# Kernel tuning notes

Hardware: AMD Instinct MI355X
Metric: run time of the kernel (lower is better)

## Reference

```python
import jax, jax.numpy as jnp
import numpy as np

# ---- static config (mirrors SynthesisLayer __init__ with chosen init_kwargs) ----
B, CIN, COUT, H, W, WDIM = 8, 512, 512, 64, 64, 512
K = 3                      # conv_kernel (not torgb)
UP, DOWN = 2, 2            # tmp_fs=128 vs in/out fs=64
TAPS = 12                  # filter_size * factor
PX0, PX1, PY0, PY1 = 9, 8, 9, 8   # from the padding formula in __init__
CLAMP = 256.0
SLOPE = 0.2
LRELU_GAIN = float(np.sqrt(2.0))
IN_CUTOFF, IN_HALFW = 16.0, 16.0
OUT_CUTOFF, OUT_HALFW = 16.0, 16.0
TMP_FS = 128.0


def _design_lowpass(numtaps, cutoff, width, fs):
    # numpy re-implementation of scipy.signal.firwin (Kaiser-window design)
    nyq = fs / 2.0
    m = np.arange(numtaps) - (numtaps - 1) / 2.0
    c = cutoff / nyq
    h = c * np.sinc(c * m)
    atten = 2.285 * (numtaps - 1) * np.pi * (width / nyq) + 7.95  # kaiser_atten
    if atten > 50:
        beta = 0.1102 * (atten - 8.7)
    elif atten > 21:
        beta = 0.5842 * (atten - 21) ** 0.4 + 0.07886 * (atten - 21)
    else:
        beta = 0.0
    h *= np.kaiser(numtaps, beta)
    h /= h.sum()
    return jnp.asarray(h, dtype=jnp.float32)


def _upfirdn2d_sep(x, f, up=1, down=1, padding=(0, 0, 0, 0), gain=1.0):
    # separable 1D filter applied along W then H; matches NVIDIA upfirdn2d ref
    C = x.shape[1]
    px0, px1, py0, py1 = padding
    f = f[::-1]  # flip_filter=False -> true convolution
    f = (f * np.sqrt(gain)).astype(x.dtype)  # gain ** (ndim/2) per 1D pass
    k = f.shape[0]
    dn = ('NCHW', 'OIHW', 'NCHW')
    # zero-upsample (trailing zeros) == lhs_dilation + (up-1) extra high pad
    kw = jnp.tile(f.reshape(1, 1, 1, k), (C, 1, 1, 1))
    x = jax.lax.conv_general_dilated(x, kw, (1, down), ((0, 0), (px0, px1 + up - 1)),
                                     lhs_dilation=(1, up), dimension_numbers=dn,
                                     feature_group_count=C)
    kh = jnp.tile(f.reshape(1, 1, k, 1), (C, 1, 1, 1))
    x = jax.lax.conv_general_dilated(x, kh, (down, 1), ((py0, py1 + up - 1), (0, 0)),
                                     lhs_dilation=(up, 1), dimension_numbers=dn,
                                     feature_group_count=C)
    return x


def _modulated_conv2d(x, w, s):
    # demodulate=True path; input_gain = rsqrt(magnitude_ema=1) = 1
    b, i, h, wid = x.shape
    o = w.shape[0]
    w = w * jax.lax.rsqrt(jnp.mean(jnp.square(w), axis=(1, 2, 3), keepdims=True))
    s = s * jax.lax.rsqrt(jnp.mean(jnp.square(s)))
    wb = w[None] * s[:, None, :, None, None]                      # [B,O,I,kh,kw]
    d = jax.lax.rsqrt(jnp.sum(jnp.square(wb), axis=(2, 3, 4)) + 1e-8)  # [B,O]
    wb = wb * d[:, :, None, None, None]
    xg = x.reshape(1, b * i, h, wid)
    wg = wb.reshape(b * o, i, K, K)
    y = jax.lax.conv_general_dilated(xg, wg, (1, 1), ((K - 1, K - 1), (K - 1, K - 1)),
                                     dimension_numbers=('NCHW', 'OIHW', 'NCHW'),
                                     feature_group_count=b)
    return y.reshape(b, o, h + K - 1, wid + K - 1)


def setup_inputs() -> dict:
    key = jax.random.key(0)
    ks = jax.random.split(key, 5)
    x = jax.random.normal(ks[0], (B, CIN, H, W), jnp.float32)
    w_lat = jax.random.normal(ks[1], (B, WDIM), jnp.float32)
    conv_w = jax.random.normal(ks[2], (COUT, CIN, K, K), jnp.float32)
    conv_b = jax.random.normal(ks[3], (COUT,), jnp.float32) * 0.1
    aff_w = jax.random.normal(ks[4], (CIN, WDIM), jnp.float32)
    aff_b = jnp.ones((CIN,), jnp.float32)  # style affine bias_init=1
    up_f = _design_lowpass(TAPS, IN_CUTOFF, 2 * IN_HALFW, TMP_FS)
    dn_f = _design_lowpass(TAPS, OUT_CUTOFF, 2 * OUT_HALFW, TMP_FS)
    return {"x": x, "w_lat": w_lat, "conv_w": conv_w, "conv_b": conv_b,
            "aff_w": aff_w, "aff_b": aff_b, "up_f": up_f, "dn_f": dn_f}


def reference(x, w_lat, conv_w, conv_b, aff_w, aff_b, up_f, dn_f):
    # affine (equalized linear, weight scale 1/sqrt(w_dim))
    styles = (w_lat @ aff_w.T) * (1.0 / np.sqrt(WDIM)) + aff_b
    y = _modulated_conv2d(x, conv_w, styles)                     # [B,O,66,66]
    # filtered_lrelu reference: bias -> clamp -> FIR up -> lrelu*gain -> clamp -> FIR down
    y = y + conv_b[None, :, None, None]
    y = jnp.clip(y, -CLAMP, CLAMP)
    y = _upfirdn2d_sep(y, up_f, up=UP, padding=(PX0, PX1, PY0, PY1), gain=UP * UP)
    y = jax.nn.leaky_relu(y, SLOPE) * LRELU_GAIN
    y = jnp.clip(y, -CLAMP, CLAMP)
    y = _upfirdn2d_sep(y, dn_f, down=DOWN)                       # [B,O,64,64]
    return y
```

## Files before the change

kernel.cpp:

```cpp
#include <hip/hip_runtime.h>
#include <stdint.h>

typedef short short8 __attribute__((ext_vector_type(8)));
typedef float f32x4 __attribute__((ext_vector_type(4)));

__device__ __forceinline__ unsigned short f2bf(float f) {
  union { float f; unsigned u; } v; v.f = f;
  unsigned u = v.u;
  u += 0x7fffu + ((u >> 16) & 1u);
  return (unsigned short)(u >> 16);
}

__device__ __forceinline__ void gl16(const void* g, void* l) {
  __builtin_amdgcn_global_load_lds(
      (__attribute__((address_space(1))) void*)(uintptr_t)g,
      (__attribute__((address_space(3))) void*)l, 16, 0, 0);
}

#define NSPAT 36992
#define PLANE 4624
#define XHP_ROWS 37152

__global__ void styles_kernel(const float* __restrict__ w_lat, const float* __restrict__ affw,
                              const float* __restrict__ affb, float* __restrict__ s) {
  int g = blockIdx.x * 256 + threadIdx.x;
  int b = g >> 9, i = g & 511;
  const float4* wl = (const float4*)(w_lat + b * 512);
  const float4* aw = (const float4*)(affw + (size_t)i * 512);
  float acc = 0.f;
#pragma unroll 4
  for (int j = 0; j < 128; ++j) {
    float4 a = wl[j], c = aw[j];
    acc += a.x * c.x + a.y * c.y + a.z * c.z + a.w * c.w;
  }
  s[g] = acc * 0.044194173824159216f + affb[i];
}

__global__ void norm_kernel(float* __restrict__ s, float* __restrict__ s2) {
  __shared__ float red[256];
  int t = threadIdx.x;
  float acc = 0.f;
  for (int e = t; e < 4096; e += 256) { float v = s[e]; acc += v * v; }
  red[t] = acc; __syncthreads();
  for (int st = 128; st > 0; st >>= 1) {
    if (t < st) red[t] += red[t + st];
    __syncthreads();
  }
  float alpha = rsqrtf(red[0] * (1.0f / 4096.0f));
  for (int e = t; e < 4096; e += 256) {
    float v = s[e] * alpha;
    s[e] = v; s2[e] = v * v;
  }
}

__global__ void rowscale_kernel(const float* __restrict__ convw, float* __restrict__ rowscale) {
  int o = blockIdx.x, t = threadIdx.x;
  const float* wr = convw + (size_t)o * 4608;
  float acc = 0.f;
  for (int e = t; e < 4608; e += 256) { float v = wr[e]; acc += v * v; }
  __shared__ float red[256];
  red[t] = acc; __syncthreads();
  for (int st = 128; st > 0; st >>= 1) {
    if (t < st) red[t] += red[t + st];
    __syncthreads();
  }
  if (t == 0) rowscale[o] = rsqrtf(red[0] * (1.0f / 4608.0f));
}

__global__ void wprep_kernel(const float* __restrict__ convw, const float* __restrict__ rowscale,
                             unsigned short* __restrict__ wbf, float* __restrict__ W2) {
  int o = blockIdx.x, t = threadIdx.x;
  float sc = rowscale[o];
  for (int i = t; i < 512; i += 256) {
    const float* wp = convw + ((size_t)o * 512 + i) * 9;
    float w9[9]; float ss = 0.f;
#pragma unroll
    for (int m = 0; m < 9; ++m) { float v = wp[m] * sc; w9[m] = v; ss += v * v; }
    W2[((size_t)o << 9) + i] = ss;
#pragma unroll
    for (int m = 0; m < 9; ++m)
      wbf[(((size_t)m * 512 + o) << 9) + i] = f2bf(w9[m]);
  }
}

__global__ void demod_kernel(const float* __restrict__ s2, const float* __restrict__ W2,
                             float* __restrict__ dbuf) {
  int g = blockIdx.x * 256 + threadIdx.x;
  int b = g >> 9, o = g & 511;
  const float4* sp = (const float4*)(s2 + b * 512);
  const float4* wp = (const float4*)(W2 + (size_t)o * 512);
  float acc = 1e-8f;
#pragma unroll 4
  for (int j = 0; j < 128; ++j) {
    float4 a = sp[j], c = wp[j];
    acc += a.x * c.x + a.y * c.y + a.z * c.z + a.w * c.w;
  }
  dbuf[g] = rsqrtf(acc);
}

__global__ void xprep_kernel(const float* __restrict__ x, const float* __restrict__ s,
                             unsigned short* __restrict__ xhp) {
  int b = blockIdx.x >> 6, h = blockIdx.x & 63;
  int t = threadIdx.x;
  __shared__ float tile[64 * 65];
  __shared__ float sv[64];
  for (int it = 0; it < 8; ++it) {
    int i0 = it * 64;
    {
      int ii = t >> 2, wseg = (t & 3) * 16;
      const float4* src = (const float4*)(x + (((size_t)(b * 512 + i0 + ii) * 64 + h) << 6) + wseg);
      float4 v0 = src[0], v1 = src[1], v2 = src[2], v3 = src[3];
      float* dst = tile + ii * 65 + wseg;
      dst[0]=v0.x; dst[1]=v0.y; dst[2]=v0.z; dst[3]=v0.w;
      dst[4]=v1.x; dst[5]=v1.y; dst[6]=v1.z; dst[7]=v1.w;
      dst[8]=v2.x; dst[9]=v2.y; dst[10]=v2.z; dst[11]=v2.w;
      dst[12]=v3.x; dst[13]=v3.y; dst[14]=v3.z; dst[15]=v3.w;
    }
    if (t < 64) sv[t] = s[b * 512 + i0 + t];
    __syncthreads();
    {
      int w = t >> 2, ic = (t & 3) * 16;
      alignas(16) unsigned short tmp[16];
#pragma unroll
      for (int k = 0; k < 16; ++k)
        tmp[k] = f2bf(tile[(ic + k) * 65 + w] * sv[ic + k]);
      unsigned short* dst = xhp + ((size_t)b * PLANE + (h + 2) * 68 + (w + 2)) * 512 + i0 + ic;
      *(short8*)dst = *(const short8*)tmp;
      *(short8*)(dst + 8) = *(const short8*)(tmp + 8);
    }
    __syncthreads();
  }
}

__global__ __launch_bounds__(256, 3) void conv_kernel(const unsigned short* __restrict__ wbf,
                                                      const unsigned short* __restrict__ xhp,
                                                      const float* __restrict__ dbuf,
                                                      const float* __restrict__ convb,
                                                      float* __restrict__ ybuf) {
  __shared__ unsigned short lds[24576];
  const int t = threadIdx.x;
  const int lane = t & 63, wid = t >> 6;

  int orig = blockIdx.y * 4 + blockIdx.x;
  int xcd = orig & 7, idx = orig >> 3;
  int wg = (xcd < 4) ? (xcd * 145 + idx) : (580 + (xcd - 4) * 144 + idx);
  const int n0 = (wg >> 2) * 128, o0 = (wg & 3) * 128;
  const int wm = wid >> 1, wn = wid & 1;

  const unsigned kc = (((unsigned)(lane & 3)) ^ ((unsigned)(lane >> 3) & 3u)) * 8u;
  const unsigned aOff0 = (unsigned)(o0 + wid * 32 + (lane >> 2)) * 512 + kc;
  const unsigned aOff1 = aOff0 + 16 * 512;
  const unsigned bOff0 = (unsigned)(n0 + wid * 32 + (lane >> 2)) * 512 + kc;
  const unsigned bOff1 = bOff0 + 16 * 512;

  const unsigned xq = ((unsigned)(lane >> 4)) ^ (((unsigned)(lane & 15) >> 1) & 3u);
  const unsigned aFo = wm * 2048 + (lane & 15) * 32 + xq * 8;
  const unsigned bFo = 4096 + wn * 2048 + (lane & 15) * 32 + xq * 8;

  f32x4 acc[4][4] = {};

#define STAGE(stp, off) do {                                           \
    const unsigned tp = (unsigned)(stp) >> 4;                          \
    const unsigned k0 = ((unsigned)(stp) & 15u) * 32u;                 \
    const unsigned aT = tp * 262144u + k0;                             \
    const unsigned bS = ((tp / 3u) * 68u + (tp % 3u)) * 512u + k0;     \
    unsigned short* la = lds + (off) + wid * 1024;                     \
    unsigned short* lb = lds + (off) + 4096 + wid * 1024;              \
    gl16(wbf + aT + aOff0, la);                                        \
    gl16(wbf + aT + aOff1, la + 512);                                  \
    gl16(xhp + bS + bOff0, lb);                                        \
    gl16(xhp + bS + bOff1, lb + 512);                                  \
  } while (0)

#define COMPUTE(rdoff) do {                                            \
    const unsigned short* aF = lds + (rdoff) + aFo;                    \
    const unsigned short* bF = lds + (rdoff) + bFo;                    \
    short8 a0 = *(const short8*)(aF + 0);                              \
    short8 a1 = *(const short8*)(aF + 512);                            \
    short8 a2 = *(const short8*)(aF + 1024);                           \
    short8 a3 = *(const short8*)(aF + 1536);                           \
    short8 b0 = *(const short8*)(bF + 0);                              \
    short8 b1 = *(const short8*)(bF + 512);                            \
    short8 b2 = *(const short8*)(bF + 1024);                           \
    short8 b3 = *(const short8*)(bF + 1536);                           \
    __builtin_amdgcn_s_setprio(1);                                     \
    acc[0][0] = __builtin_amdgcn_mfma_f32_16x16x32_bf16(a0, b0, acc[0][0], 0, 0, 0); \
    acc[0][1] = __builtin_amdgcn_mfma_f32_16x16x32_bf16(a0, b1, acc[0][1], 0, 0, 0); \
    acc[0][2] = __builtin_amdgcn_mfma_f32_16x16x32_bf16(a0, b2, acc[0][2], 0, 0, 0); \
    acc[0][3] = __builtin_amdgcn_mfma_f32_16x16x32_bf16(a0, b3, acc[0][3], 0, 0, 0); \
    acc[1][0] = __builtin_amdgcn_mfma_f32_16x16x32_bf16(a1, b0, acc[1][0], 0, 0, 0); \
    acc[1][1] = __builtin_amdgcn_mfma_f32_16x16x32_bf16(a1, b1, acc[1][1], 0, 0, 0); \
    acc[1][2] = __builtin_amdgcn_mfma_f32_16x16x32_bf16(a1, b2, acc[1][2], 0, 0, 0); \
    acc[1][3] = __builtin_amdgcn_mfma_f32_16x16x32_bf16(a1, b3, acc[1][3], 0, 0, 0); \
    acc[2][0] = __builtin_amdgcn_mfma_f32_16x16x32_bf16(a2, b0, acc[2][0], 0, 0, 0); \
    acc[2][1] = __builtin_amdgcn_mfma_f32_16x16x32_bf16(a2, b1, acc[2][1], 0, 0, 0); \
    acc[2][2] = __builtin_amdgcn_mfma_f32_16x16x32_bf16(a2, b2, acc[2][2], 0, 0, 0); \
    acc[2][3] = __builtin_amdgcn_mfma_f32_16x16x32_bf16(a2, b3, acc[2][3], 0, 0, 0); \
    acc[3][0] = __builtin_amdgcn_mfma_f32_16x16x32_bf16(a3, b0, acc[3][0], 0, 0, 0); \
    acc[3][1] = __builtin_amdgcn_mfma_f32_16x16x32_bf16(a3, b1, acc[3][1], 0, 0, 0); \
    acc[3][2] = __builtin_amdgcn_mfma_f32_16x16x32_bf16(a3, b2, acc[3][2], 0, 0, 0); \
    acc[3][3] = __builtin_amdgcn_mfma_f32_16x16x32_bf16(a3, b3, acc[3][3], 0, 0, 0); \
    __builtin_amdgcn_s_setprio(0);                                     \
  } while (0)

  STAGE(0, 0u);
  STAGE(1, 8192u);

  unsigned rd = 0, wr2 = 16384;
  for (int step = 0; step < 143; ++step) {
    asm volatile("s_waitcnt vmcnt(4)" ::: "memory");
    __builtin_amdgcn_s_barrier();
    asm volatile("" ::: "memory");
    if (step < 142) STAGE(step + 2, wr2);
    COMPUTE(rd);
    asm volatile("" ::: "memory");
    rd += 8192;  if (rd == 24576) rd = 0;
    wr2 += 8192; if (wr2 == 24576) wr2 = 0;
  }
  asm volatile("s_waitcnt vmcnt(0)" ::: "memory");
  __builtin_amdgcn_s_barrier();
  asm volatile("" ::: "memory");
  COMPUTE(rd);
#undef STAGE
#undef COMPUTE

  const int col = lane & 15;
  const int rbase = (lane >> 4) * 4;
#pragma unroll
  for (int ni = 0; ni < 4; ++ni) {
    const unsigned n = (unsigned)(n0 + wn * 64 + ni * 16 + col);
    const unsigned b = n / 4624u;
    const float* dr = dbuf + b * 512;
#pragma unroll
    for (int mi = 0; mi < 4; ++mi) {
      const int ob = o0 + wm * 64 + mi * 16 + rbase;
#pragma unroll
      for (int j = 0; j < 4; ++j) {
        const int o = ob + j;
        float v = acc[mi][ni][j] * dr[o] + convb[o];
        v = fminf(fmaxf(v, -256.f), 256.f);
        ybuf[(size_t)o * NSPAT + n] = v;
      }
    }
  }
}

__global__ __launch_bounds__(256, 4) void updown_kernel(const float* __restrict__ ybuf,
                                                        const float* __restrict__ upf,
                                                        const float* __restrict__ dnf,
                                                        float* __restrict__ out) {
  __shared__ float sm[9880];
  float* uhB = sm;
  float* uB  = sm + 5016;
  float* dvT = sm + 5016;

  const int blk = blockIdx.x;
  const int half = blk & 1, ch = blk >> 1;
  const int o = ch & 511, b = ch >> 9;
  const float* ybase = ybuf + (size_t)o * NSPAT + b * PLANE;
  const int t = threadIdx.x;
  const int uc0 = half * 32 - 4;

  float f2[12], g[12];
#pragma unroll
  for (int m = 0; m < 12; ++m) { f2[m] = upf[11 - m] * 2.0f; g[m] = dnf[11 - m]; }

  for (int u = t; u < 726; u += 256) {
    int p = u / 11, q = u - p * 11;
    int gc = uc0 + 4 * q;
    f32x4 v = {0.f, 0.f, 0.f, 0.f};
    if (gc >= 0 && gc < 66) {
      v = *(const f32x4*)(ybase + p * 68 + gc);
#pragma unroll
      for (int j = 0; j < 4; ++j)
        if (gc + j >= 66) v[j] = 0.f;
    }
    *(f32x4*)(uB + p * 44 + 4 * q) = v;
  }
  __syncthreads();

  for (int u = t; u < 1254; u += 256) {
    int p = u / 19, cq = u - p * 19;
    const float* ur = uB + p * 44 + 2 * cq;
    float R0 = ur[0], R1 = ur[1], R2 = ur[2], R3 = ur[3], R4 = ur[4], R5 = ur[5], R6 = ur[6];
    f32x4 o4;
    o4[0] = f2[1]*R0 + f2[3]*R1 + f2[5]*R2 + f2[7]*R3 + f2[9]*R4 + f2[11]*R5;
    o4[1] = f2[0]*R0 + f2[2]*R1 + f2[4]*R2 + f2[6]*R3 + f2[8]*R4 + f2[10]*R5;
    o4[2] = f2[1]*R1 + f2[3]*R2 + f2[5]*R3 + f2[7]*R4 + f2[9]*R5 + f2[11]*R6;
    o4[3] = f2[0]*R1 + f2[2]*R2 + f2[4]*R3 + f2[6]*R4 + f2[8]*R5 + f2[10]*R6;
    *(f32x4*)(uhB + p * 76 + 4 * cq) = o4;
  }
  __syncthreads();

  if (t < 225) {
    const int cl = t % 75, sg = t / 75;
    const int s0 = sg * 22;
    const int ttg0 = 2 * s0;
    float R[32];
#pragma unroll
    for (int k = 0; k < 32; ++k) {
      int j = s0 - 4 + k;
      R[k] = (j >= 0 && j < 66) ? uhB[j * 76 + cl] : 0.f;
    }
    float dv[22];
#pragma unroll
    for (int m = 0; m < 22; ++m) dv[m] = 0.f;
#pragma unroll
    for (int k = 0; k < 54; ++k) {
      const int kb = k >> 1;
      float z;
      if (k & 1)
        z = f2[0]*R[kb] + f2[2]*R[kb+1] + f2[4]*R[kb+2] + f2[6]*R[kb+3] + f2[8]*R[kb+4] + f2[10]*R[kb+5];
      else
        z = f2[1]*R[kb] + f2[3]*R[kb+1] + f2[5]*R[kb+2] + f2[7]*R[kb+3] + f2[9]*R[kb+4] + f2[11]*R[kb+5];
      z = (z > 0.f ? z : 0.2f * z) * 1.4142135623730951f;
      z = fminf(fmaxf(z, -256.f), 256.f);
      if (ttg0 + k >= 138) z = 0.f;
      const int mlo = (k < 11) ? 0 : ((k - 10) >> 1);
      const int mhi = ((k >> 1) < 21) ? (k >> 1) : 21;
#pragma unroll
      for (int m = mlo; m <= mhi; ++m)
        dv[m] += g[k - 2 * m] * z;
    }
#pragma unroll
    for (int m = 0; m < 22; ++m) {
      const int s = s0 + m;
      if (s < 64) dvT[s * 76 + cl] = dv[m];
    }
  }
  __syncthreads();

  {
    const int s = t >> 2, rq = t & 3;
    const float* dr = dvT + s * 76 + 16 * rq;
    f32x4 dd[7];
#pragma unroll
    for (int i = 0; i < 7; ++i) dd[i] = *(const f32x4*)(dr + 4 * i);
    float D[28];
#pragma unroll
    for (int i = 0; i < 7; ++i) {
      D[4*i+0] = dd[i][0]; D[4*i+1] = dd[i][1]; D[4*i+2] = dd[i][2]; D[4*i+3] = dd[i][3];
    }
    f32x4 o0, o1;
#pragma unroll
    for (int m = 0; m < 8; ++m) {
      float v = g[0]*D[2*m] + g[1]*D[2*m+1] + g[2]*D[2*m+2] + g[3]*D[2*m+3]
              + g[4]*D[2*m+4] + g[5]*D[2*m+5] + g[6]*D[2*m+6] + g[7]*D[2*m+7]
              + g[8]*D[2*m+8] + g[9]*D[2*m+9] + g[10]*D[2*m+10] + g[11]*D[2*m+11];
      if (m < 4) o0[m] = v; else o1[m - 4] = v;
    }
    float* ob = out + (((size_t)(b * 512 + o)) << 12) + s * 64 + half * 32 + 8 * rq;
    *(f32x4*)ob = o0;
    *(f32x4*)(ob + 4) = o1;
  }
}

extern "C" void kernel_launch(void* const* d_in, const int* in_sizes, int n_in,
                              void* d_out, int out_size, void* d_ws, size_t ws_size,
                              hipStream_t stream) {
  const float* x     = (const float*)d_in[0];
  const float* w_lat = (const float*)d_in[1];
  const float* convw = (const float*)d_in[2];
  const float* convb = (const float*)d_in[3];
  const float* affw  = (const float*)d_in[4];
  const float* affb  = (const float*)d_in[5];
  const float* upf   = (const float*)d_in[6];
  const float* dnf   = (const float*)d_in[7];
  float* out = (float*)d_out;

  char* ws = (char*)d_ws;
  float* s         = (float*)(ws + 0);
  float* s2        = (float*)(ws + 16384);
  float* rowscale  = (float*)(ws + 32768);
  float* W2        = (float*)(ws + 34816);
  float* dbuf      = (float*)(ws + 1083392);
  unsigned short* wbf = (unsigned short*)(ws + 1099776);
  unsigned short* xhp = (unsigned short*)(ws + 5818368);
  float* ybuf      = (float*)(ws + 43862016);

  styles_kernel<<<16, 256, 0, stream>>>(w_lat, affw, affb, s);
  norm_kernel<<<1, 256, 0, stream>>>(s, s2);
  rowscale_kernel<<<512, 256, 0, stream>>>(convw, rowscale);
  wprep_kernel<<<512, 256, 0, stream>>>(convw, rowscale, wbf, W2);
  demod_kernel<<<16, 256, 0, stream>>>(s2, W2, dbuf);

  hipMemsetAsync(xhp, 0, (size_t)XHP_ROWS * 512 * 2, stream);
  xprep_kernel<<<512, 256, 0, stream>>>(x, s, xhp);

  dim3 cgrid(4, 289);
  conv_kernel<<<cgrid, 256, 0, stream>>>(wbf, xhp, dbuf, convb, ybuf);

  updown_kernel<<<8192, 256, 0, stream>>>(ybuf, upf, dnf, out);
}
```

Measured before the change: 379.7 us.

## Switch conv GEMM to two-stage double buffer with 64-wide K tiles

Replaces the three-stage, 32-wide-K LDS ring in the modulated conv GEMM with a two-stage ping-pong buffer that loads 64 K-elements per stage. Each iteration now issues eight global-to-LDS loads and runs two MFMA sub-blocks, halving the number of barriers and loop iterations. The LDS footprint grows to 64 KB of dynamic shared memory, so launch bounds drop from 3 to 2 blocks per CU. The wait now drains all outstanding loads before each barrier, which may expose more memory latency than the previous deeper pipeline did.

Result: faster. 362.1 us (-4.6%).

```diff
diff --git a/kernel.cpp b/kernel.cpp
--- a/kernel.cpp
+++ b/kernel.cpp
@@ -132,12 +132,12 @@
   }
 }
 
-__global__ __launch_bounds__(256, 3) void conv_kernel(const unsigned short* __restrict__ wbf,
+__global__ __launch_bounds__(256, 2) void conv_kernel(const unsigned short* __restrict__ wbf,
                                                       const unsigned short* __restrict__ xhp,
                                                       const float* __restrict__ dbuf,
                                                       const float* __restrict__ convb,
                                                       float* __restrict__ ybuf) {
-  __shared__ unsigned short lds[24576];
+  extern __shared__ unsigned short lds[];
   const int t = threadIdx.x;
   const int lane = t & 63, wid = t >> 6;
 
@@ -147,43 +147,44 @@
   const int n0 = (wg >> 2) * 128, o0 = (wg & 3) * 128;
   const int wm = wid >> 1, wn = wid & 1;
 
-  const unsigned kc = (((unsigned)(lane & 3)) ^ ((unsigned)(lane >> 3) & 3u)) * 8u;
-  const unsigned aOff0 = (unsigned)(o0 + wid * 32 + (lane >> 2)) * 512 + kc;
-  const unsigned aOff1 = aOff0 + 16 * 512;
-  const unsigned bOff0 = (unsigned)(n0 + wid * 32 + (lane >> 2)) * 512 + kc;
-  const unsigned bOff1 = bOff0 + 16 * 512;
+  const unsigned kcq = (((unsigned)(lane & 3)) ^ ((unsigned)(lane >> 3) & 3u)) * 8u;
+  const unsigned aSrc = (unsigned)(o0 + wid * 16 + (lane >> 2)) * 512 + kcq;
+  const unsigned bSrc = (unsigned)(n0 + wid * 16 + (lane >> 2)) * 512 + kcq;
 
   const unsigned xq = ((unsigned)(lane >> 4)) ^ (((unsigned)(lane & 15) >> 1) & 3u);
-  const unsigned aFo = wm * 2048 + (lane & 15) * 32 + xq * 8;
-  const unsigned bFo = 4096 + wn * 2048 + (lane & 15) * 32 + xq * 8;
+  const unsigned aRd = (unsigned)(wm * 64 + (lane & 15)) * 32 + xq * 8;
+  const unsigned bRd = (unsigned)(wn * 64 + (lane & 15)) * 32 + xq * 8;
 
   f32x4 acc[4][4] = {};
 
-#define STAGE(stp, off) do {                                           \
-    const unsigned tp = (unsigned)(stp) >> 4;                          \
-    const unsigned k0 = ((unsigned)(stp) & 15u) * 32u;                 \
-    const unsigned aT = tp * 262144u + k0;                             \
-    const unsigned bS = ((tp / 3u) * 68u + (tp % 3u)) * 512u + k0;     \
-    unsigned short* la = lds + (off) + wid * 1024;                     \
-    unsigned short* lb = lds + (off) + 4096 + wid * 1024;              \
-    gl16(wbf + aT + aOff0, la);                                        \
-    gl16(wbf + aT + aOff1, la + 512);                                  \
-    gl16(xhp + bS + bOff0, lb);                                        \
-    gl16(xhp + bS + bOff1, lb + 512);                                  \
+#define STAGE(kt, bufb) do {                                            \
+    const unsigned kti = (unsigned)(kt);                                \
+    const unsigned tap = kti >> 3, k0e = (kti & 7u) * 64u;              \
+    const unsigned aB = tap * 262144u + k0e;                            \
+    const unsigned bB = ((tap / 3u) * 68u + (tap % 3u)) * 512u + k0e;   \
+    unsigned short* lb = lds + (bufb) * 16384 + wid * 512;              \
+    gl16(wbf + aB + aSrc,              lb);                             \
+    gl16(wbf + aB + aSrc + 32768,      lb + 2048);                      \
+    gl16(wbf + aB + 32 + aSrc,         lb + 4096);                      \
+    gl16(wbf + aB + 32 + aSrc + 32768, lb + 6144);                      \
+    gl16(xhp + bB + bSrc,              lb + 8192);                      \
+    gl16(xhp + bB + bSrc + 32768,      lb + 10240);                     \
+    gl16(xhp + bB + 32 + bSrc,         lb + 12288);                     \
+    gl16(xhp + bB + 32 + bSrc + 32768, lb + 14336);                     \
   } while (0)
 
-#define COMPUTE(rdoff) do {                                            \
-    const unsigned short* aF = lds + (rdoff) + aFo;                    \
-    const unsigned short* bF = lds + (rdoff) + bFo;                    \
-    short8 a0 = *(const short8*)(aF + 0);                              \
-    short8 a1 = *(const short8*)(aF + 512);                            \
-    short8 a2 = *(const short8*)(aF + 1024);                           \
-    short8 a3 = *(const short8*)(aF + 1536);                           \
-    short8 b0 = *(const short8*)(bF + 0);                              \
-    short8 b1 = *(const short8*)(bF + 512);                            \
-    short8 b2 = *(const short8*)(bF + 1024);                           \
-    short8 b3 = *(const short8*)(bF + 1536);                           \
-    __builtin_amdgcn_s_setprio(1);                                     \
+#define COMPUTE_KK(bufb, kk) do {                                       \
+    const unsigned short* aF = lds + (bufb) * 16384 + (kk) * 4096 + aRd;        \
+    const unsigned short* bF = lds + (bufb) * 16384 + 8192 + (kk) * 4096 + bRd; \
+    short8 a0 = *(const short8*)(aF + 0);                               \
+    short8 a1 = *(const short8*)(aF + 512);                             \
+    short8 a2 = *(const short8*)(aF + 1024);                            \
+    short8 a3 = *(const short8*)(aF + 1536);                            \
+    short8 b0 = *(const short8*)(bF + 0);                               \
+    short8 b1 = *(const short8*)(bF + 512);                             \
+    short8 b2 = *(const short8*)(bF + 1024);                            \
+    short8 b3 = *(const short8*)(bF + 1536);                            \
+    __builtin_amdgcn_s_setprio(1);                                      \
     acc[0][0] = __builtin_amdgcn_mfma_f32_16x16x32_bf16(a0, b0, acc[0][0], 0, 0, 0); \
     acc[0][1] = __builtin_amdgcn_mfma_f32_16x16x32_bf16(a0, b1, acc[0][1], 0, 0, 0); \
     acc[0][2] = __builtin_amdgcn_mfma_f32_16x16x32_bf16(a0, b2, acc[0][2], 0, 0, 0); \
@@ -200,29 +201,23 @@
     acc[3][1] = __builtin_amdgcn_mfma_f32_16x16x32_bf16(a3, b1, acc[3][1], 0, 0, 0); \
     acc[3][2] = __builtin_amdgcn_mfma_f32_16x16x32_bf16(a3, b2, acc[3][2], 0, 0, 0); \
     acc[3][3] = __builtin_amdgcn_mfma_f32_16x16x32_bf16(a3, b3, acc[3][3], 0, 0, 0); \
-    __builtin_amdgcn_s_setprio(0);                                     \
+    __builtin_amdgcn_s_setprio(0);                                      \
   } while (0)
 
-  STAGE(0, 0u);
-  STAGE(1, 8192u);
-
-  unsigned rd = 0, wr2 = 16384;
-  for (int step = 0; step < 143; ++step) {
-    asm volatile("s_waitcnt vmcnt(4)" ::: "memory");
+  STAGE(0, 0);
+
+  for (int k = 0; k < 72; ++k) {
+    asm volatile("s_waitcnt vmcnt(0)" ::: "memory");
     __builtin_amdgcn_s_barrier();
     asm volatile("" ::: "memory");
-    if (step < 142) STAGE(step + 2, wr2);
-    COMPUTE(rd);
+    if (k < 71) STAGE(k + 1, (k + 1) & 1);
+    __builtin_amdgcn_sched_barrier(0);
+    COMPUTE_KK(k & 1, 0);
+    COMPUTE_KK(k & 1, 1);
     asm volatile("" ::: "memory");
-    rd += 8192;  if (rd == 24576) rd = 0;
-    wr2 += 8192; if (wr2 == 24576) wr2 = 0;
-  }
-  asm volatile("s_waitcnt vmcnt(0)" ::: "memory");
-  __builtin_amdgcn_s_barrier();
-  asm volatile("" ::: "memory");
-  COMPUTE(rd);
+  }
 #undef STAGE
-#undef COMPUTE
+#undef COMPUTE_KK
 
   const int col = lane & 15;
   const int rbase = (lane >> 4) * 4;
@@ -388,7 +383,7 @@
   xprep_kernel<<<512, 256, 0, stream>>>(x, s, xhp);
 
   dim3 cgrid(4, 289);
-  conv_kernel<<<cgrid, 256, 0, stream>>>(wbf, xhp, dbuf, convb, ybuf);
+  conv_kernel<<<cgrid, 256, 65536, stream>>>(wbf, xhp, dbuf, convb, ybuf);
 
   updown_kernel<<<8192, 256, 0, stream>>>(ybuf, upf, dnf, out);
 }
```
